# Performance work log

Measured on AMD Instinct MI355X. Metric: run time of the kernel, lower is better.

Reference implementation:

```python
import jax, jax.numpy as jnp
import numpy as np

N_NODES = 100000
N_EDGES = 800000
HIDDEN = 128
BN_EPS = 1e-5


def setup_inputs() -> dict:
    key = jax.random.key(0)
    k1, k2, k3 = jax.random.split(key, 3)
    x = jax.random.normal(k1, (N_NODES, HIDDEN), dtype=jnp.float32)
    edge_index = jax.random.randint(k2, (2, N_EDGES), 0, N_NODES, dtype=jnp.int64)
    # Glorot-style init for the GCN linear weight
    W = jax.random.normal(k3, (HIDDEN, HIDDEN), dtype=jnp.float32) / np.sqrt(HIDDEN)
    b = jnp.zeros((HIDDEN,), dtype=jnp.float32)
    gamma = jnp.ones((HIDDEN,), dtype=jnp.float32)
    beta = jnp.zeros((HIDDEN,), dtype=jnp.float32)
    return {"x": x, "edge_index": edge_index, "W": W, "b": b, "gamma": gamma, "beta": beta}


def reference(x, edge_index, W, b, gamma, beta):
    N = x.shape[0]
    xw = x @ W  # [N, d] linear transform first (PyG order)

    # add self-loops
    loops = jnp.arange(N, dtype=edge_index.dtype)
    row = jnp.concatenate([edge_index[0], loops])  # source
    col = jnp.concatenate([edge_index[1], loops])  # target

    # symmetric degree normalization on A~ = A + I
    deg = jax.ops.segment_sum(jnp.ones_like(col, dtype=x.dtype), col, num_segments=N)
    dinv = jax.lax.rsqrt(jnp.maximum(deg, 1.0))  # deg >= 1 due to self-loops
    norm = dinv[row] * dinv[col]  # [E+N]

    # gather -> scale -> scatter-add aggregation
    msgs = xw[row] * norm[:, None]  # [E+N, d]
    agg = jax.ops.segment_sum(msgs, col, num_segments=N) + b  # [N, d]

    # BatchNorm1d (batch statistics, biased variance) + ReLU; Dropout is identity (eval)
    mean = jnp.mean(agg, axis=0)
    var = jnp.var(agg, axis=0)
    h = (agg - mean) * jax.lax.rsqrt(var + BN_EPS) * gamma + beta
    return jax.nn.relu(h)
```

## Files before the change

### kernel.cpp

```cpp
#include <hip/hip_runtime.h>
#include <cstddef>

#define HIDDEN 128
#define BN_EPS 1e-5f
#define KS 136
#define BKT 64

typedef __attribute__((ext_vector_type(8))) short short8;
typedef __attribute__((ext_vector_type(4))) float float4v;
typedef __attribute__((ext_vector_type(4))) unsigned uint4v;

__device__ inline unsigned bf16_rne(float f) {
    unsigned u = __float_as_uint(f);
    return (u + 0x7fff + ((u >> 16) & 1)) >> 16;
}
__device__ inline unsigned pack2_bf16(float a, float b) {
    return bf16_rne(a) | (bf16_rne(b) << 16);
}

__global__ void k_count(const int* __restrict__ col, const int* __restrict__ row,
                        int* __restrict__ cnt, int* bucket, int E) {
    int base = (blockIdx.x * 256 + threadIdx.x) * 4;
    if (base + 3 < E) {
        int4 c = *(const int4*)&col[base];
        int4 r = *(const int4*)&row[base];
        int p0 = atomicAdd(&cnt[c.x], 1);
        int p1 = atomicAdd(&cnt[c.y], 1);
        int p2 = atomicAdd(&cnt[c.z], 1);
        int p3 = atomicAdd(&cnt[c.w], 1);
        if (p0 < BKT) bucket[(size_t)c.x * BKT + p0] = r.x;
        if (p1 < BKT) bucket[(size_t)c.y * BKT + p1] = r.y;
        if (p2 < BKT) bucket[(size_t)c.z * BKT + p2] = r.z;
        if (p3 < BKT) bucket[(size_t)c.w * BKT + p3] = r.w;
    } else {
        for (int k = 0; k < 4; ++k) {
            int e = base + k;
            if (e < E) {
                int c = col[e];
                int r = row[e];
                int p = atomicAdd(&cnt[c], 1);
                if (p < BKT) bucket[(size_t)c * BKT + p] = r;
            }
        }
    }
}

__global__ __launch_bounds__(256) void k_gemm(const float* __restrict__ x,
                                              const float* __restrict__ W,
                                              const int* __restrict__ cnt,
                                              unsigned short* __restrict__ xus, int N) {
    __shared__ unsigned short lA[128 * KS];
    __shared__ unsigned short lB[128 * KS];
    int tid = threadIdx.x;
    int row0 = blockIdx.x * 128;
    int wv = tid >> 6;
    int lane = tid & 63;
    int l15 = lane & 15;
    int lq = lane >> 4;

    for (int it = 0; it < 16; ++it) {
        int idx4 = it * 256 + tid;
        int m = idx4 >> 5, c4 = idx4 & 31;
        int grow = row0 + m;
        float4 v = make_float4(0.f, 0.f, 0.f, 0.f);
        if (grow < N) v = ((const float4*)x)[(size_t)grow * 32 + c4];
        uint2 pk;
        pk.x = pack2_bf16(v.x, v.y);
        pk.y = pack2_bf16(v.z, v.w);
        *(uint2*)&lA[m * KS + c4 * 4] = pk;
    }
    for (int it = 0; it < 16; ++it) {
        int idx4 = it * 256 + tid;
        int k = idx4 >> 5, n4 = idx4 & 31;
        float4 v = ((const float4*)W)[(size_t)k * 32 + n4];
        int n = n4 * 4;
        lB[(n + 0) * KS + k] = (unsigned short)bf16_rne(v.x);
        lB[(n + 1) * KS + k] = (unsigned short)bf16_rne(v.y);
        lB[(n + 2) * KS + k] = (unsigned short)bf16_rne(v.z);
        lB[(n + 3) * KS + k] = (unsigned short)bf16_rne(v.w);
    }
    __syncthreads();

    float4v acc[2][8];
#pragma unroll
    for (int i = 0; i < 2; ++i)
#pragma unroll
        for (int j = 0; j < 8; ++j) acc[i][j] = (float4v){0.f, 0.f, 0.f, 0.f};

#pragma unroll
    for (int kc = 0; kc < 4; ++kc) {
        int ko = kc * 32 + lq * 8;
        short8 a0 = *(const short8*)&lA[(wv * 32 + l15) * KS + ko];
        short8 a1 = *(const short8*)&lA[(wv * 32 + 16 + l15) * KS + ko];
        short8 bfr[8];
#pragma unroll
        for (int nt = 0; nt < 8; ++nt)
            bfr[nt] = *(const short8*)&lB[(nt * 16 + l15) * KS + ko];
#pragma unroll
        for (int nt = 0; nt < 8; ++nt) {
            acc[0][nt] = __builtin_amdgcn_mfma_f32_16x16x32_bf16(a0, bfr[nt], acc[0][nt], 0, 0, 0);
            acc[1][nt] = __builtin_amdgcn_mfma_f32_16x16x32_bf16(a1, bfr[nt], acc[1][nt], 0, 0, 0);
        }
    }

    __syncthreads();

#pragma unroll
    for (int mt = 0; mt < 2; ++mt) {
#pragma unroll
        for (int reg = 0; reg < 4; ++reg) {
            int rl = wv * 32 + mt * 16 + lq * 4 + reg;
            int r = row0 + rl;
            float d = 0.f;
            if (r < N) d = rsqrtf((float)(cnt[r] + 1));
#pragma unroll
            for (int nt = 0; nt < 8; ++nt)
                lA[rl * KS + nt * 16 + l15] = (unsigned short)bf16_rne(acc[mt][nt][reg] * d);
        }
    }
    __syncthreads();

    for (int it = 0; it < 8; ++it) {
        int idx = it * 256 + tid;
        int r = idx >> 4, c16 = idx & 15;
        int grow = row0 + r;
        if (grow < N) {
            uint4v v = *(const uint4v*)&lA[r * KS + c16 * 8];
            *((uint4v*)(xus + (size_t)grow * 128) + c16) = v;
        }
    }
}

__global__ __launch_bounds__(256) void k_gather(const unsigned* __restrict__ xu,
                                                const int* __restrict__ cnt,
                                                const float* __restrict__ b,
                                                unsigned* aggsrc,
                                                float* __restrict__ bn, int N) {
    int tid = threadIdx.x;
    int lane = tid & 63;
    int w = (blockIdx.x * 256 + tid) >> 6;
    int nw = (gridDim.x * 256) >> 6;
    float2 bb = ((const float2*)b)[lane];
    float2 s = make_float2(0.f, 0.f), qq = make_float2(0.f, 0.f);

    const int* bkt = (const int*)aggsrc;

    int i = w;
    int deg = 0;
    unsigned uself = 0;
    int pf[16];
#pragma unroll
    for (int k = 0; k < 16; ++k) pf[k] = 0;
    if (i < N) {
        deg = cnt[i];
        uself = xu[(size_t)i * 64 + lane];
        const int4* bp = (const int4*)(bkt + (size_t)i * BKT);
        int4 q0 = bp[0], q1 = bp[1], q2 = bp[2], q3 = bp[3];
        pf[0] = q0.x; pf[1] = q0.y; pf[2]  = q0.z; pf[3]  = q0.w;
        pf[4] = q1.x; pf[5] = q1.y; pf[6]  = q1.z; pf[7]  = q1.w;
        pf[8] = q2.x; pf[9] = q2.y; pf[10] = q2.z; pf[11] = q2.w;
        pf[12] = q3.x; pf[13] = q3.y; pf[14] = q3.z; pf[15] = q3.w;
    }

    while (i < N) {
        int inext = i + nw;
        int ndeg = 0;
        unsigned nself = 0;
        int npf[16];
#pragma unroll
        for (int k = 0; k < 16; ++k) npf[k] = 0;
        if (inext < N) {
            ndeg = cnt[inext];
            nself = xu[(size_t)inext * 64 + lane];
            const int4* bp = (const int4*)(bkt + (size_t)inext * BKT);
            int4 q0 = bp[0], q1 = bp[1], q2 = bp[2], q3 = bp[3];
            npf[0] = q0.x; npf[1] = q0.y; npf[2]  = q0.z; npf[3]  = q0.w;
            npf[4] = q1.x; npf[5] = q1.y; npf[6]  = q1.z; npf[7]  = q1.w;
            npf[8] = q2.x; npf[9] = q2.y; npf[10] = q2.z; npf[11] = q2.w;
            npf[12] = q3.x; npf[13] = q3.y; npf[14] = q3.z; npf[15] = q3.w;
        }

        int d = __builtin_amdgcn_readfirstlane(deg);
        if (d > BKT) d = BKT;
        float di = rsqrtf((float)(d + 1));
        float ax = __uint_as_float(uself << 16);
        float ay = __uint_as_float(uself & 0xffff0000u);

        if (d > 0) {
            unsigned u[8];
#pragma unroll
            for (int k = 0; k < 8; ++k) {
                int rk = (k < d) ? pf[k] : pf[0];
                u[k] = xu[(size_t)rk * 64 + lane];
            }
#pragma unroll
            for (int k = 0; k < 8; ++k) {
                unsigned uu = (k < d) ? u[k] : 0u;
                ax += __uint_as_float(uu << 16);
                ay += __uint_as_float(uu & 0xffff0000u);
            }
        }
        if (d > 8) {
            unsigned u[8];
#pragma unroll
            for (int k = 0; k < 8; ++k) {
                int rk = (8 + k < d) ? pf[8 + k] : pf[0];
                u[k] = xu[(size_t)rk * 64 + lane];
            }
#pragma unroll
            for (int k = 0; k < 8; ++k) {
                unsigned uu = (8 + k < d) ? u[k] : 0u;
                ax += __uint_as_float(uu << 16);
                ay += __uint_as_float(uu & 0xffff0000u);
            }
        }
        if (d > 16) {
            const int* bp = bkt + (size_t)i * BKT;
            int j = 16;
            for (; j + 8 <= d; j += 8) {
                int r0 = bp[j + 0], r1 = bp[j + 1], r2 = bp[j + 2], r3 = bp[j + 3];
                int r4 = bp[j + 4], r5 = bp[j + 5], r6 = bp[j + 6], r7 = bp[j + 7];
                unsigned u0 = xu[(size_t)r0 * 64 + lane];
                unsigned u1 = xu[(size_t)r1 * 64 + lane];
                unsigned u2 = xu[(size_t)r2 * 64 + lane];
                unsigned u3 = xu[(size_t)r3 * 64 + lane];
                unsigned u4 = xu[(size_t)r4 * 64 + lane];
                unsigned u5 = xu[(size_t)r5 * 64 + lane];
                unsigned u6 = xu[(size_t)r6 * 64 + lane];
                unsigned u7 = xu[(size_t)r7 * 64 + lane];
                ax += __uint_as_float(u0 << 16) + __uint_as_float(u1 << 16)
                    + __uint_as_float(u2 << 16) + __uint_as_float(u3 << 16);
                ay += __uint_as_float(u0 & 0xffff0000u) + __uint_as_float(u1 & 0xffff0000u)
                    + __uint_as_float(u2 & 0xffff0000u) + __uint_as_float(u3 & 0xffff0000u);
                ax += __uint_as_float(u4 << 16) + __uint_as_float(u5 << 16)
                    + __uint_as_float(u6 << 16) + __uint_as_float(u7 << 16);
                ay += __uint_as_float(u4 & 0xffff0000u) + __uint_as_float(u5 & 0xffff0000u)
                    + __uint_as_float(u6 & 0xffff0000u) + __uint_as_float(u7 & 0xffff0000u);
            }
            if (j < d) {
                int last = d - 1;
                int r[7];
#pragma unroll
                for (int k = 0; k < 7; ++k) {
                    int jk = j + k;
                    r[k] = bp[jk < d ? jk : last];
                }
                unsigned u[7];
#pragma unroll
                for (int k = 0; k < 7; ++k) u[k] = xu[(size_t)r[k] * 64 + lane];
#pragma unroll
                for (int k = 0; k < 7; ++k) {
                    unsigned uu = (j + k < d) ? u[k] : 0u;
                    ax += __uint_as_float(uu << 16);
                    ay += __uint_as_float(uu & 0xffff0000u);
                }
            }
        }

        float ox = fmaf(ax, di, bb.x);
        float oy = fmaf(ay, di, bb.y);
        aggsrc[(size_t)i * 64 + lane] = pack2_bf16(ox, oy);
        s.x += ox;
        s.y += oy;
        qq.x = fmaf(ox, ox, qq.x);
        qq.y = fmaf(oy, oy, qq.y);

        i = inext;
        deg = ndeg;
        uself = nself;
#pragma unroll
        for (int k = 0; k < 16; ++k) pf[k] = npf[k];
    }

    __shared__ float ssum[HIDDEN];
    __shared__ float ssq[HIDDEN];
    if (tid < HIDDEN) { ssum[tid] = 0.f; ssq[tid] = 0.f; }
    __syncthreads();
    atomicAdd(&ssum[2 * lane],     s.x);
    atomicAdd(&ssum[2 * lane + 1], s.y);
    atomicAdd(&ssq[2 * lane],      qq.x);
    atomicAdd(&ssq[2 * lane + 1],  qq.y);
    __syncthreads();
    if (tid < HIDDEN) {
        atomicAdd(&bn[tid],          ssum[tid]);
        atomicAdd(&bn[HIDDEN + tid], ssq[tid]);
    }
}

__global__ __launch_bounds__(256) void k_apply(const unsigned* __restrict__ agg,
                                               float* __restrict__ out,
                                               const float* __restrict__ bn,
                                               const float* __restrict__ gamma,
                                               const float* __restrict__ beta,
                                               int total8, float invN) {
    __shared__ float sc[HIDDEN], sh[HIDDEN];
    int tid = threadIdx.x;
    if (tid < HIDDEN) {
        float mean = bn[tid] * invN;
        float var = bn[HIDDEN + tid] * invN - mean * mean;
        float inv = rsqrtf(var + BN_EPS);
        float g = gamma[tid] * inv;
        sc[tid] = g;
        sh[tid] = beta[tid] - mean * g;
    }
    __syncthreads();
    int idx = blockIdx.x * 256 + tid;
    if (idx < total8) {
        uint2 u = ((const uint2*)agg)[idx];
        int c = (idx & 31) * 4;
        float4 v;
        v.x = __uint_as_float(u.x << 16);
        v.y = __uint_as_float(u.x & 0xffff0000u);
        v.z = __uint_as_float(u.y << 16);
        v.w = __uint_as_float(u.y & 0xffff0000u);
        v.x = fmaxf(fmaf(v.x, sc[c],     sh[c]),     0.f);
        v.y = fmaxf(fmaf(v.y, sc[c + 1], sh[c + 1]), 0.f);
        v.z = fmaxf(fmaf(v.z, sc[c + 2], sh[c + 2]), 0.f);
        v.w = fmaxf(fmaf(v.w, sc[c + 3], sh[c + 3]), 0.f);
        ((float4*)out)[idx] = v;
    }
}

extern "C" void kernel_launch(void* const* d_in, const int* in_sizes, int n_in,
                              void* d_out, int out_size, void* d_ws, size_t ws_size,
                              hipStream_t stream) {
    const float* x     = (const float*)d_in[0];
    const int*   edges = (const int*)d_in[1];
    const float* W     = (const float*)d_in[2];
    const float* b     = (const float*)d_in[3];
    const float* gamma = (const float*)d_in[4];
    const float* beta  = (const float*)d_in[5];
    float* out = (float*)d_out;

    int N = in_sizes[0] / HIDDEN;
    int E = in_sizes[1] / 2;
    const int* row = edges;
    const int* col = edges + E;

    char* p = (char*)d_ws;
    unsigned* xu  = (unsigned*)p; p += (size_t)N * 64 * sizeof(unsigned);
    unsigned* agg = (unsigned*)p; p += (size_t)N * 64 * sizeof(unsigned);
    int*   cnt    = (int*)p;   p += (size_t)N * sizeof(int);
    float* bn     = (float*)p; p += 256 * sizeof(float);

    size_t zbytes = (size_t)N * sizeof(int) + 256 * sizeof(float);

    dim3 blk(256);
    hipMemsetAsync(cnt, 0, zbytes, stream);
    k_count<<<dim3((E + 1023) / 1024), blk, 0, stream>>>(col, row, cnt, (int*)agg, E);
    k_gemm<<<dim3((N + 127) / 128), blk, 0, stream>>>(x, W, cnt, (unsigned short*)xu, N);
    k_gather<<<dim3(2048), blk, 0, stream>>>(xu, cnt, b, agg, bn, N);
    int total8 = N * 32;
    k_apply<<<dim3((total8 + 255) / 256), blk, 0, stream>>>(agg, out, bn, gamma, beta,
                                                            total8, 1.0f / (float)N);
}
```

Measured before the change: 287.1 us.

## Merge count and GEMM kernels into one launch, apply source degree scaling in gather

The edge-count/bucket kernel and the bf16 MFMA GEMM are combined into a single launch whose blocks are interleaved between the two roles. This lets the atomic-heavy counting run alongside the compute-heavy GEMM. To remove the GEMM's dependency on degree counts, the source-side rsqrt(deg) scaling moves out of the GEMM epilogue into the gather, which now loads cnt[src] per edge and uses an FMA. The cost is an extra random 4-byte load and an rsqrt per neighbour in the gather. Rounding also changes slightly, because the bf16 values are now stored unscaled.

```diff
diff --git a/kernel.cpp b/kernel.cpp
--- a/kernel.cpp
+++ b/kernel.cpp
@@ -18,41 +18,56 @@
     return bf16_rne(a) | (bf16_rne(b) << 16);
 }
 
-__global__ void k_count(const int* __restrict__ col, const int* __restrict__ row,
-                        int* __restrict__ cnt, int* bucket, int E) {
-    int base = (blockIdx.x * 256 + threadIdx.x) * 4;
-    if (base + 3 < E) {
-        int4 c = *(const int4*)&col[base];
-        int4 r = *(const int4*)&row[base];
-        int p0 = atomicAdd(&cnt[c.x], 1);
-        int p1 = atomicAdd(&cnt[c.y], 1);
-        int p2 = atomicAdd(&cnt[c.z], 1);
-        int p3 = atomicAdd(&cnt[c.w], 1);
-        if (p0 < BKT) bucket[(size_t)c.x * BKT + p0] = r.x;
-        if (p1 < BKT) bucket[(size_t)c.y * BKT + p1] = r.y;
-        if (p2 < BKT) bucket[(size_t)c.z * BKT + p2] = r.z;
-        if (p3 < BKT) bucket[(size_t)c.w * BKT + p3] = r.w;
-    } else {
-        for (int k = 0; k < 4; ++k) {
-            int e = base + k;
-            if (e < E) {
-                int c = col[e];
-                int r = row[e];
-                int p = atomicAdd(&cnt[c], 1);
-                if (p < BKT) bucket[(size_t)c * BKT + p] = r;
-            }
-        }
-    }
-}
-
-__global__ __launch_bounds__(256) void k_gemm(const float* __restrict__ x,
-                                              const float* __restrict__ W,
-                                              const int* __restrict__ cnt,
-                                              unsigned short* __restrict__ xus, int N) {
+__global__ __launch_bounds__(256) void k_front(const float* __restrict__ x,
+                                               const float* __restrict__ W,
+                                               unsigned short* __restrict__ xus,
+                                               const int* __restrict__ col,
+                                               const int* __restrict__ row,
+                                               int* __restrict__ cnt, int* bucket,
+                                               int N, int E, int GB, int CB) {
     __shared__ unsigned short lA[128 * KS];
     __shared__ unsigned short lB[128 * KS];
+    int bid = blockIdx.x;
     int tid = threadIdx.x;
-    int row0 = blockIdx.x * 128;
+    int m2 = 2 * (GB < CB ? GB : CB);
+    bool isGemm;
+    int rid;
+    if (bid < m2) {
+        isGemm = (bid & 1);
+        rid = bid >> 1;
+    } else {
+        isGemm = (GB > CB);
+        rid = (m2 >> 1) + (bid - m2);
+    }
+
+    if (!isGemm) {
+        int base = (rid * 256 + tid) * 4;
+        if (base + 3 < E) {
+            int4 c = *(const int4*)&col[base];
+            int4 r = *(const int4*)&row[base];
+            int p0 = atomicAdd(&cnt[c.x], 1);
+            int p1 = atomicAdd(&cnt[c.y], 1);
+            int p2 = atomicAdd(&cnt[c.z], 1);
+            int p3 = atomicAdd(&cnt[c.w], 1);
+            if (p0 < BKT) bucket[(size_t)c.x * BKT + p0] = r.x;
+            if (p1 < BKT) bucket[(size_t)c.y * BKT + p1] = r.y;
+            if (p2 < BKT) bucket[(size_t)c.z * BKT + p2] = r.z;
+            if (p3 < BKT) bucket[(size_t)c.w * BKT + p3] = r.w;
+        } else {
+            for (int k = 0; k < 4; ++k) {
+                int e = base + k;
+                if (e < E) {
+                    int c = col[e];
+                    int r = row[e];
+                    int p = atomicAdd(&cnt[c], 1);
+                    if (p < BKT) bucket[(size_t)c * BKT + p] = r;
+                }
+            }
+        }
+        return;
+    }
+
+    int row0 = rid * 128;
     int wv = tid >> 6;
     int lane = tid & 63;
     int l15 = lane & 15;
@@ -110,12 +125,9 @@
 #pragma unroll
         for (int reg = 0; reg < 4; ++reg) {
             int rl = wv * 32 + mt * 16 + lq * 4 + reg;
-            int r = row0 + rl;
-            float d = 0.f;
-            if (r < N) d = rsqrtf((float)(cnt[r] + 1));
 #pragma unroll
             for (int nt = 0; nt < 8; ++nt)
-                lA[rl * KS + nt * 16 + l15] = (unsigned short)bf16_rne(acc[mt][nt][reg] * d);
+                lA[rl * KS + nt * 16 + l15] = (unsigned short)bf16_rne(acc[mt][nt][reg]);
         }
     }
     __syncthreads();
@@ -183,76 +195,81 @@
         int d = __builtin_amdgcn_readfirstlane(deg);
         if (d > BKT) d = BKT;
         float di = rsqrtf((float)(d + 1));
-        float ax = __uint_as_float(uself << 16);
-        float ay = __uint_as_float(uself & 0xffff0000u);
+        float ax = __uint_as_float(uself << 16) * di;
+        float ay = __uint_as_float(uself & 0xffff0000u) * di;
 
         if (d > 0) {
+            int rks[8];
             unsigned u[8];
-#pragma unroll
-            for (int k = 0; k < 8; ++k) {
-                int rk = (k < d) ? pf[k] : pf[0];
-                u[k] = xu[(size_t)rk * 64 + lane];
-            }
+            float ds[8];
+#pragma unroll
+            for (int k = 0; k < 8; ++k) rks[k] = (k < d) ? pf[k] : pf[0];
+#pragma unroll
+            for (int k = 0; k < 8; ++k) u[k] = xu[(size_t)rks[k] * 64 + lane];
+#pragma unroll
+            for (int k = 0; k < 8; ++k) ds[k] = rsqrtf((float)(cnt[rks[k]] + 1));
 #pragma unroll
             for (int k = 0; k < 8; ++k) {
                 unsigned uu = (k < d) ? u[k] : 0u;
-                ax += __uint_as_float(uu << 16);
-                ay += __uint_as_float(uu & 0xffff0000u);
+                ax = fmaf(__uint_as_float(uu << 16), ds[k], ax);
+                ay = fmaf(__uint_as_float(uu & 0xffff0000u), ds[k], ay);
             }
         }
         if (d > 8) {
+            int rks[8];
             unsigned u[8];
-#pragma unroll
-            for (int k = 0; k < 8; ++k) {
-                int rk = (8 + k < d) ? pf[8 + k] : pf[0];
-                u[k] = xu[(size_t)rk * 64 + lane];
-            }
+            float ds[8];
+#pragma unroll
+            for (int k = 0; k < 8; ++k) rks[k] = (8 + k < d) ? pf[8 + k] : pf[0];
+#pragma unroll
+            for (int k = 0; k < 8; ++k) u[k] = xu[(size_t)rks[k] * 64 + lane];
+#pragma unroll
+            for (int k = 0; k < 8; ++k) ds[k] = rsqrtf((float)(cnt[rks[k]] + 1));
 #pragma unroll
             for (int k = 0; k < 8; ++k) {
                 unsigned uu = (8 + k < d) ? u[k] : 0u;
-                ax += __uint_as_float(uu << 16);
-                ay += __uint_as_float(uu & 0xffff0000u);
+                ax = fmaf(__uint_as_float(uu << 16), ds[k], ax);
+                ay = fmaf(__uint_as_float(uu & 0xffff0000u), ds[k], ay);
             }
         }
         if (d > 16) {
             const int* bp = bkt + (size_t)i * BKT;
             int j = 16;
             for (; j + 8 <= d; j += 8) {
-                int r0 = bp[j + 0], r1 = bp[j + 1], r2 = bp[j + 2], r3 = bp[j + 3];
-                int r4 = bp[j + 4], r5 = bp[j + 5], r6 = bp[j + 6], r7 = bp[j + 7];
-                unsigned u0 = xu[(size_t)r0 * 64 + lane];
-                unsigned u1 = xu[(size_t)r1 * 64 + lane];
-                unsigned u2 = xu[(size_t)r2 * 64 + lane];
-                unsigned u3 = xu[(size_t)r3 * 64 + lane];
-                unsigned u4 = xu[(size_t)r4 * 64 + lane];
-                unsigned u5 = xu[(size_t)r5 * 64 + lane];
-                unsigned u6 = xu[(size_t)r6 * 64 + lane];
-                unsigned u7 = xu[(size_t)r7 * 64 + lane];
-                ax += __uint_as_float(u0 << 16) + __uint_as_float(u1 << 16)
-                    + __uint_as_float(u2 << 16) + __uint_as_float(u3 << 16);
-                ay += __uint_as_float(u0 & 0xffff0000u) + __uint_as_float(u1 & 0xffff0000u)
-                    + __uint_as_float(u2 & 0xffff0000u) + __uint_as_float(u3 & 0xffff0000u);
-                ax += __uint_as_float(u4 << 16) + __uint_as_float(u5 << 16)
-                    + __uint_as_float(u6 << 16) + __uint_as_float(u7 << 16);
-                ay += __uint_as_float(u4 & 0xffff0000u) + __uint_as_float(u5 & 0xffff0000u)
-                    + __uint_as_float(u6 & 0xffff0000u) + __uint_as_float(u7 & 0xffff0000u);
+                int rr[8];
+                unsigned u[8];
+                float ds[8];
+#pragma unroll
+                for (int k = 0; k < 8; ++k) rr[k] = bp[j + k];
+#pragma unroll
+                for (int k = 0; k < 8; ++k) u[k] = xu[(size_t)rr[k] * 64 + lane];
+#pragma unroll
+                for (int k = 0; k < 8; ++k) ds[k] = rsqrtf((float)(cnt[rr[k]] + 1));
+#pragma unroll
+                for (int k = 0; k < 8; ++k) {
+                    ax = fmaf(__uint_as_float(u[k] << 16), ds[k], ax);
+                    ay = fmaf(__uint_as_float(u[k] & 0xffff0000u), ds[k], ay);
+                }
             }
             if (j < d) {
                 int last = d - 1;
-                int r[7];
+                int rr[7];
+                unsigned u[7];
+                float ds[7];
 #pragma unroll
                 for (int k = 0; k < 7; ++k) {
                     int jk = j + k;
-                    r[k] = bp[jk < d ? jk : last];
+                    rr[k] = bp[jk < d ? jk : last];
                 }
-                unsigned u[7];
-#pragma unroll
-                for (int k = 0; k < 7; ++k) u[k] = xu[(size_t)r[k] * 64 + lane];
+#pragma unroll
+                for (int k = 0; k < 7; ++k) u[k] = xu[(size_t)rr[k] * 64 + lane];
+#pragma unroll
+                for (int k = 0; k < 7; ++k) ds[k] = rsqrtf((float)(cnt[rr[k]] + 1));
 #pragma unroll
                 for (int k = 0; k < 7; ++k) {
                     unsigned uu = (j + k < d) ? u[k] : 0u;
-                    ax += __uint_as_float(uu << 16);
-                    ay += __uint_as_float(uu & 0xffff0000u);
+                    ax = fmaf(__uint_as_float(uu << 16), ds[k], ax);
+                    ay = fmaf(__uint_as_float(uu & 0xffff0000u), ds[k], ay);
                 }
             }
         }
@@ -345,10 +362,13 @@
 
     size_t zbytes = (size_t)N * sizeof(int) + 256 * sizeof(float);
 
+    int GB = (N + 127) / 128;
+    int CB = (E + 1023) / 1024;
+
     dim3 blk(256);
     hipMemsetAsync(cnt, 0, zbytes, stream);
-    k_count<<<dim3((E + 1023) / 1024), blk, 0, stream>>>(col, row, cnt, (int*)agg, E);
-    k_gemm<<<dim3((N + 127) / 128), blk, 0, stream>>>(x, W, cnt, (unsigned short*)xu, N);
+    k_front<<<dim3(GB + CB), blk, 0, stream>>>(x, W, (unsigned short*)xu, col, row,
+                                               cnt, (int*)agg, N, E, GB, CB);
     k_gather<<<dim3(2048), blk, 0, stream>>>(xu, cnt, b, agg, bn, N);
     int total8 = N * 32;
     k_apply<<<dim3((total8 + 255) / 256), blk, 0, stream>>>(agg, out, bn, gamma, beta,
```

Result: faster. 262.6 us (-8.5%).
